# Optimization experiments

Measured on AMD Instinct MI355X. Metric: run time of the kernel, lower is better.

## Reference

```python
import jax, jax.numpy as jnp
import numpy as np

N_NODES = 100000
N_EDGES = 1600000
IN_CH = 256
OUT_CH = 128


def setup_inputs() -> dict:
    key = jax.random.key(0)
    k1, k2, k3, k4, k5, k6 = jax.random.split(key, 6)
    x = jax.random.normal(k1, (N_NODES, IN_CH), dtype=jnp.float32)
    edge_src = jax.random.randint(k2, (N_EDGES,), 0, N_NODES, dtype=jnp.int32)
    edge_dst = jax.random.randint(k3, (N_EDGES,), 0, N_NODES, dtype=jnp.int32)
    edge_weight = jax.random.uniform(k4, (N_EDGES,), dtype=jnp.float32)
    # Linear params (torch nn.Linear: y = x @ W.T + b)
    W = jax.random.normal(k5, (OUT_CH, IN_CH), dtype=jnp.float32) * (1.0 / np.sqrt(IN_CH))
    b = jax.random.normal(k6, (OUT_CH,), dtype=jnp.float32) * 0.01
    return {"x": x, "edge_src": edge_src, "edge_dst": edge_dst,
            "edge_weight": edge_weight, "W": W, "b": b}


def reference(x, edge_src, edge_dst, edge_weight, W, b):
    # Linear projection: [N, in] -> [N, out]
    h = x @ W.T + b
    # spmm sum aggregation: out[d] = sum_{e: dst(e)=d} w_e * h[src(e)]
    msgs = h[edge_src] * edge_weight[:, None]  # [E, out]
    out = jax.ops.segment_sum(msgs, edge_dst, num_segments=N_NODES)
    return out
```

## Files before the change

kernel.cpp:

```cpp
#include <hip/hip_runtime.h>
#include <hip/hip_bf16.h>

#define IN_CH 256
#define OUT_CH 128
#define BKT_SHIFT 7
#define BKT_SIZE 128
#define MAXNB 1024
#define K3_CHUNK 8192
#define MAXBLK 256
#define BATCH 3072
#define CAPP 4096

using bf16x8 = __attribute__((ext_vector_type(8))) __bf16;
using f32x16 = __attribute__((ext_vector_type(16))) float;
using f32x4  = __attribute__((ext_vector_type(4))) float;
using f32x2  = __attribute__((ext_vector_type(2))) float;

__device__ __forceinline__ unsigned int f2bf(float f) {
    union { float f; unsigned u; } v; v.f = f;
    unsigned r = v.u + 0x7fffu + ((v.u >> 16) & 1u);
    return r >> 16;
}
__device__ __forceinline__ float bf2f(unsigned short u) {
    union { unsigned u; float f; } v; v.u = ((unsigned)u) << 16;
    return v.f;
}

__global__ void __launch_bounds__(256) prep_w(const float* __restrict__ W,
                                              unsigned short* __restrict__ Wfrag) {
    const int flat = blockIdx.x * 256 + threadIdx.x;
    const int l = flat & 63;
    const int ks = (flat >> 6) & 15;
    const int c = flat >> 10;
    const int row = c * 32 + (l & 31);
    const int col0 = ks * 16 + 8 * (l >> 5);
    const float* src = W + (size_t)row * IN_CH + col0;
    uint4 o;
    o.x = f2bf(src[0]) | (f2bf(src[1]) << 16);
    o.y = f2bf(src[2]) | (f2bf(src[3]) << 16);
    o.z = f2bf(src[4]) | (f2bf(src[5]) << 16);
    o.w = f2bf(src[6]) | (f2bf(src[7]) << 16);
    *reinterpret_cast<uint4*>(Wfrag + (size_t)flat * 8) = o;
}

__global__ void __launch_bounds__(256) linear_mfma(
    const float* __restrict__ x, const unsigned short* __restrict__ Wfrag,
    const float* __restrict__ b, unsigned short* __restrict__ h, int n_nodes) {
    const int tid = threadIdx.x;
    const int w = tid >> 6, l = tid & 63;
    const int l31 = l & 31, lh = l >> 5;
    const int node0 = blockIdx.x * 128 + w * 32;

    int arow = node0 + l31;
    if (arow > n_nodes - 1) arow = n_nodes - 1;
    const float* xrow = x + (size_t)arow * IN_CH + 8 * lh;
    const uint4* wf = reinterpret_cast<const uint4*>(Wfrag);

    f32x16 acc0 = {}, acc1 = {}, acc2 = {}, acc3 = {};

#pragma unroll 4
    for (int ks = 0; ks < 16; ++ks) {
        float4 a0 = *reinterpret_cast<const float4*>(xrow + ks * 16);
        float4 a1 = *reinterpret_cast<const float4*>(xrow + ks * 16 + 4);
        bf16x8 af;
        af[0] = (__bf16)a0.x; af[1] = (__bf16)a0.y;
        af[2] = (__bf16)a0.z; af[3] = (__bf16)a0.w;
        af[4] = (__bf16)a1.x; af[5] = (__bf16)a1.y;
        af[6] = (__bf16)a1.z; af[7] = (__bf16)a1.w;

        uint4 bw0 = wf[(0 * 16 + ks) * 64 + l];
        uint4 bw1 = wf[(1 * 16 + ks) * 64 + l];
        uint4 bw2 = wf[(2 * 16 + ks) * 64 + l];
        uint4 bw3 = wf[(3 * 16 + ks) * 64 + l];

        acc0 = __builtin_amdgcn_mfma_f32_32x32x16_bf16(af, __builtin_bit_cast(bf16x8, bw0), acc0, 0, 0, 0);
        acc1 = __builtin_amdgcn_mfma_f32_32x32x16_bf16(af, __builtin_bit_cast(bf16x8, bw1), acc1, 0, 0, 0);
        acc2 = __builtin_amdgcn_mfma_f32_32x32x16_bf16(af, __builtin_bit_cast(bf16x8, bw2), acc2, 0, 0, 0);
        acc3 = __builtin_amdgcn_mfma_f32_32x32x16_bf16(af, __builtin_bit_cast(bf16x8, bw3), acc3, 0, 0, 0);
    }

    const float bias0 = b[0 + l31], bias1 = b[32 + l31], bias2 = b[64 + l31], bias3 = b[96 + l31];
#pragma unroll
    for (int reg = 0; reg < 16; ++reg) {
        const int r = (reg & 3) + 8 * (reg >> 2) + 4 * lh;
        const int node = node0 + r;
        if (node < n_nodes) {
            unsigned short* hp = h + (size_t)node * OUT_CH;
            __bf16 t0 = (__bf16)(acc0[reg] + bias0);
            __bf16 t1 = (__bf16)(acc1[reg] + bias1);
            __bf16 t2 = (__bf16)(acc2[reg] + bias2);
            __bf16 t3 = (__bf16)(acc3[reg] + bias3);
            hp[0 + l31]  = __builtin_bit_cast(unsigned short, t0);
            hp[32 + l31] = __builtin_bit_cast(unsigned short, t1);
            hp[64 + l31] = __builtin_bit_cast(unsigned short, t2);
            hp[96 + l31] = __builtin_bit_cast(unsigned short, t3);
        }
    }
}

__global__ void __launch_bounds__(512) k1_hist(
    const int* __restrict__ edge_dst, int* __restrict__ bh, int n_edges, int nb) {
    __shared__ int hist[MAXNB];
    const int t = threadIdx.x;
    const int blk = blockIdx.x;
    for (int i = t; i < MAXNB; i += 512) hist[i] = 0;
    __syncthreads();
    const int base = blk * K3_CHUNK;
#pragma unroll
    for (int j = 0; j < K3_CHUNK / 512; ++j) {
        int e = base + j * 512 + t;
        if (e < n_edges) atomicAdd(&hist[edge_dst[e] >> BKT_SHIFT], 1);
    }
    __syncthreads();
    for (int i = t; i < nb; i += 512) bh[i * MAXBLK + blk] = hist[i];
}

__global__ void __launch_bounds__(256) k2a_scan_cols(
    const int* __restrict__ bh, int* __restrict__ offs, int* __restrict__ total,
    int nblk) {
    __shared__ int sd[256];
    const int t = threadIdx.x;
    const int bkt = blockIdx.x;
    int val = (t < nblk) ? bh[bkt * MAXBLK + t] : 0;
    sd[t] = val;
    __syncthreads();
    for (int s = 1; s < 256; s <<= 1) {
        int y = (t >= s) ? sd[t - s] : 0;
        __syncthreads();
        sd[t] += y;
        __syncthreads();
    }
    offs[bkt * MAXBLK + t] = sd[t] - val;
    if (t == 255) total[bkt] = sd[255];
}

__global__ void __launch_bounds__(256) k2b_scan_base(
    const int* __restrict__ total, int* __restrict__ base, int nb) {
    __shared__ int sd[256];
    const int t = threadIdx.x;
    int v[4];
    int loc = 0;
#pragma unroll
    for (int k = 0; k < 4; ++k) {
        int idx = t * 4 + k;
        v[k] = (idx < nb) ? total[idx] : 0;
        loc += v[k];
    }
    sd[t] = loc;
    __syncthreads();
    for (int s = 1; s < 256; s <<= 1) {
        int y = (t >= s) ? sd[t - s] : 0;
        __syncthreads();
        sd[t] += y;
        __syncthreads();
    }
    int run = sd[t] - loc;
#pragma unroll
    for (int k = 0; k < 4; ++k) {
        int idx = t * 4 + k;
        if (idx < nb) base[idx] = run;
        run += v[k];
    }
    if (t == 255) base[nb] = sd[255];
}

__global__ void __launch_bounds__(512) k3_bin(
    const int* __restrict__ edge_src, const int* __restrict__ edge_dst,
    const float* __restrict__ edge_weight,
    const int* __restrict__ offs, const int* __restrict__ base,
    unsigned long long* __restrict__ records, int n_edges, int nb) {
    __shared__ unsigned long long staged[K3_CHUNK];
    __shared__ int hist[MAXNB];
    __shared__ int cur[MAXNB];
    __shared__ int gbase[MAXNB];
    __shared__ int sd[512];

    const int t = threadIdx.x;
    const int blk = blockIdx.x;
    const int ebase = blk * K3_CHUNK;
    const int count = min(K3_CHUNK, n_edges - ebase);

    for (int i = t; i < MAXNB; i += 512) hist[i] = 0;
    __syncthreads();
#pragma unroll
    for (int j = 0; j < K3_CHUNK / 512; ++j) {
        int e = ebase + j * 512 + t;
        if (e < n_edges) atomicAdd(&hist[edge_dst[e] >> BKT_SHIFT], 1);
    }
    __syncthreads();
    int h0 = hist[2 * t], h1 = hist[2 * t + 1];
    int loc = h0 + h1;
    sd[t] = loc;
    __syncthreads();
    for (int s = 1; s < 512; s <<= 1) {
        int y = (t >= s) ? sd[t - s] : 0;
        __syncthreads();
        sd[t] += y;
        __syncthreads();
    }
    int excl = sd[t] - loc;
    cur[2 * t] = excl;
    cur[2 * t + 1] = excl + h0;
    if (2 * t < nb)     gbase[2 * t]     = base[2 * t]     + offs[(2 * t) * MAXBLK + blk]     - excl;
    if (2 * t + 1 < nb) gbase[2 * t + 1] = base[2 * t + 1] + offs[(2 * t + 1) * MAXBLK + blk] - (excl + h0);
    __syncthreads();
#pragma unroll
    for (int j = 0; j < K3_CHUNK / 512; ++j) {
        int e = ebase + j * 512 + t;
        if (e < n_edges) {
            int d = edge_dst[e];
            int bkt = d >> BKT_SHIFT;
            unsigned int wbits = f2bf(edge_weight[e]);
            unsigned long long rec = ((unsigned long long)wbits << 48) |
                                     ((unsigned long long)bkt << 24) |
                                     ((unsigned long long)(d & (BKT_SIZE - 1)) << 17) |
                                     (unsigned int)edge_src[e];
            int pos = atomicAdd(&cur[bkt], 1);
            staged[pos] = rec;
        }
    }
    __syncthreads();
    for (int i = t; i < count; i += 512) {
        unsigned long long r = staged[i];
        int bkt = (int)((r >> 24) & 1023u);
        records[gbase[bkt] + i] = r;
    }
}

__global__ void __launch_bounds__(512) k4_agg(
    const unsigned short* __restrict__ h, const unsigned long long* __restrict__ records,
    const int* __restrict__ base, float* __restrict__ out, int n_nodes) {
    __shared__ unsigned long long sorted[CAPP];
    __shared__ int hist[BKT_SIZE];
    __shared__ int cur[BKT_SIZE];
    __shared__ int pstart[BKT_SIZE];
    __shared__ int sd[BKT_SIZE];
    __shared__ int ptot;

    const int t = threadIdx.x;
    const int bkt = blockIdx.x;
    const int w = t >> 6, lane = t & 63;
    const int rbeg = base[bkt], rend = base[bkt + 1];

    float acc[16][2];
#pragma unroll
    for (int d = 0; d < 16; ++d) { acc[d][0] = 0.f; acc[d][1] = 0.f; }

    for (int b0 = rbeg; b0 < rend; b0 += BATCH) {
        const int cnt = min(BATCH, rend - b0);
        __syncthreads();
        unsigned long long r[6];
#pragma unroll
        for (int j = 0; j < 6; ++j) {
            const int o = j * 512 + t;
            r[j] = (o < cnt) ? records[b0 + o] : 0ull;
        }
        if (t < BKT_SIZE) hist[t] = 0;
        __syncthreads();
#pragma unroll
        for (int j = 0; j < 6; ++j) {
            const int o = j * 512 + t;
            if (o < cnt) atomicAdd(&hist[(unsigned)(r[j] >> 17) & 127u], 1);
        }
        __syncthreads();
        if (t < BKT_SIZE) sd[t] = (hist[t] + 7) & ~7;
        __syncthreads();
        for (int s = 1; s < BKT_SIZE; s <<= 1) {
            int y = 0;
            if (t < BKT_SIZE && t >= s) y = sd[t - s];
            __syncthreads();
            if (t < BKT_SIZE) sd[t] += y;
            __syncthreads();
        }
        if (t < BKT_SIZE) {
            const int e = sd[t] - ((hist[t] + 7) & ~7);
            pstart[t] = e;
            cur[t] = e;
        }
        if (t == BKT_SIZE - 1) ptot = sd[BKT_SIZE - 1];
        __syncthreads();
        const int pt = ptot;
        for (int i = t; i < pt; i += 512) sorted[i] = 0ull;
        __syncthreads();
#pragma unroll
        for (int j = 0; j < 6; ++j) {
            const int o = j * 512 + t;
            if (o < cnt) {
                const int dl = (int)((unsigned)(r[j] >> 17) & 127u);
                const int pos = atomicAdd(&cur[dl], 1);
                sorted[pos] = r[j];
            }
        }
        __syncthreads();
#pragma unroll
        for (int d = 0; d < 16; ++d) {
            const int dl = w * 16 + d;
            const int s0 = pstart[dl];
            const int s1 = s0 + hist[dl];
            float a0 = 0.f, a1 = 0.f;
            for (int i = s0; i < s1; i += 8) {
                unsigned int hv[8];
                float wt[8];
#pragma unroll
                for (int j = 0; j < 8; ++j) {
                    const unsigned long long rr = sorted[i + j];
                    const unsigned lo = __builtin_amdgcn_readfirstlane((unsigned)rr);
                    const unsigned hi = __builtin_amdgcn_readfirstlane((unsigned)(rr >> 32));
                    wt[j] = __builtin_bit_cast(float, hi & 0xFFFF0000u);
                    const unsigned* hp = reinterpret_cast<const unsigned*>(
                        h + (size_t)(lo & 0x1FFFFu) * OUT_CH);
                    hv[j] = hp[lane];
                }
#pragma unroll
                for (int j = 0; j < 8; ++j) {
                    a0 += wt[j] * __builtin_bit_cast(float, hv[j] << 16);
                    a1 += wt[j] * __builtin_bit_cast(float, hv[j] & 0xFFFF0000u);
                }
            }
            acc[d][0] += a0;
            acc[d][1] += a1;
        }
    }

#pragma unroll
    for (int d = 0; d < 16; ++d) {
        const int node = bkt * BKT_SIZE + w * 16 + d;
        if (node < n_nodes) {
            f32x2 v = {acc[d][0], acc[d][1]};
            __builtin_nontemporal_store(
                v, reinterpret_cast<f32x2*>(out + (size_t)node * OUT_CH + 2 * lane));
        }
    }
}

extern "C" void kernel_launch(void* const* d_in, const int* in_sizes, int n_in,
                              void* d_out, int out_size, void* d_ws, size_t ws_size,
                              hipStream_t stream) {
    const float* x           = (const float*)d_in[0];
    const int*   edge_src    = (const int*)d_in[1];
    const int*   edge_dst    = (const int*)d_in[2];
    const float* edge_weight = (const float*)d_in[3];
    const float* W           = (const float*)d_in[4];
    const float* b           = (const float*)d_in[5];
    float* out = (float*)d_out;

    const int n_nodes = in_sizes[0] / IN_CH;
    const int n_edges = in_sizes[1];
    const int nb = (n_nodes + BKT_SIZE - 1) / BKT_SIZE;
    const int nblk = (n_edges + K3_CHUNK - 1) / K3_CHUNK;

    unsigned long long* records = (unsigned long long*)d_ws;
    unsigned short* h  = (unsigned short*)(records + n_edges);
    int* bh    = (int*)(h + (size_t)n_nodes * OUT_CH);
    int* offs  = bh + MAXNB * MAXBLK;
    int* total = offs + MAXNB * MAXBLK;
    int* base  = total + MAXNB;
    unsigned short* Wfrag = (unsigned short*)(base + MAXNB + 2);

    prep_w<<<16, 256, 0, stream>>>(W, Wfrag);
    linear_mfma<<<(n_nodes + 127) / 128, 256, 0, stream>>>(x, Wfrag, b, h, n_nodes);
    k1_hist<<<nblk, 512, 0, stream>>>(edge_dst, bh, n_edges, nb);
    k2a_scan_cols<<<nb, 256, 0, stream>>>(bh, offs, total, nblk);
    k2b_scan_base<<<1, 256, 0, stream>>>(total, base, nb);
    k3_bin<<<nblk, 512, 0, stream>>>(edge_src, edge_dst, edge_weight,
                                     offs, base, records, n_edges, nb);
    k4_agg<<<nb, 512, 0, stream>>>(h, records, base, out, n_nodes);
}
```

Baseline: 136.7 us.

## Split aggregation buckets across two blocks and stage W in LDS

The aggregation kernel now launches two blocks per 128-node bucket. Each block reads every record in the bucket but keeps only those whose destination falls in its 64-node half, which doubles the block count and parallelism at the cost of reading the records twice. The linear kernel moves to 512 threads and 256 nodes per block, and copies the 64 KB of W fragments into LDS once per block instead of loading them from global memory in every wave. The larger LDS footprint may limit how many linear blocks fit per CU.

```diff
diff --git a/kernel.cpp b/kernel.cpp
--- a/kernel.cpp
+++ b/kernel.cpp
@@ -5,6 +5,7 @@
 #define OUT_CH 128
 #define BKT_SHIFT 7
 #define BKT_SIZE 128
+#define BSUB 64
 #define MAXNB 1024
 #define K3_CHUNK 8192
 #define MAXBLK 256
@@ -43,18 +44,25 @@
     *reinterpret_cast<uint4*>(Wfrag + (size_t)flat * 8) = o;
 }
 
-__global__ void __launch_bounds__(256) linear_mfma(
+__global__ void __launch_bounds__(512) linear_mfma(
     const float* __restrict__ x, const unsigned short* __restrict__ Wfrag,
     const float* __restrict__ b, unsigned short* __restrict__ h, int n_nodes) {
+    __shared__ uint4 wlds[4096];
     const int tid = threadIdx.x;
     const int w = tid >> 6, l = tid & 63;
     const int l31 = l & 31, lh = l >> 5;
-    const int node0 = blockIdx.x * 128 + w * 32;
+    const int node0 = blockIdx.x * 256 + w * 32;
+
+    {
+        const uint4* wfg = reinterpret_cast<const uint4*>(Wfrag);
+#pragma unroll
+        for (int j = 0; j < 8; ++j) wlds[j * 512 + tid] = wfg[j * 512 + tid];
+    }
+    __syncthreads();
 
     int arow = node0 + l31;
     if (arow > n_nodes - 1) arow = n_nodes - 1;
     const float* xrow = x + (size_t)arow * IN_CH + 8 * lh;
-    const uint4* wf = reinterpret_cast<const uint4*>(Wfrag);
 
     f32x16 acc0 = {}, acc1 = {}, acc2 = {}, acc3 = {};
 
@@ -68,10 +76,10 @@
         af[4] = (__bf16)a1.x; af[5] = (__bf16)a1.y;
         af[6] = (__bf16)a1.z; af[7] = (__bf16)a1.w;
 
-        uint4 bw0 = wf[(0 * 16 + ks) * 64 + l];
-        uint4 bw1 = wf[(1 * 16 + ks) * 64 + l];
-        uint4 bw2 = wf[(2 * 16 + ks) * 64 + l];
-        uint4 bw3 = wf[(3 * 16 + ks) * 64 + l];
+        uint4 bw0 = wlds[(0 * 16 + ks) * 64 + l];
+        uint4 bw1 = wlds[(1 * 16 + ks) * 64 + l];
+        uint4 bw2 = wlds[(2 * 16 + ks) * 64 + l];
+        uint4 bw3 = wlds[(3 * 16 + ks) * 64 + l];
 
         acc0 = __builtin_amdgcn_mfma_f32_32x32x16_bf16(af, __builtin_bit_cast(bf16x8, bw0), acc0, 0, 0, 0);
         acc1 = __builtin_amdgcn_mfma_f32_32x32x16_bf16(af, __builtin_bit_cast(bf16x8, bw1), acc1, 0, 0, 0);
@@ -231,70 +239,71 @@
     const unsigned short* __restrict__ h, const unsigned long long* __restrict__ records,
     const int* __restrict__ base, float* __restrict__ out, int n_nodes) {
     __shared__ unsigned long long sorted[CAPP];
-    __shared__ int hist[BKT_SIZE];
-    __shared__ int cur[BKT_SIZE];
-    __shared__ int pstart[BKT_SIZE];
-    __shared__ int sd[BKT_SIZE];
+    __shared__ int hist[BSUB];
+    __shared__ int cur[BSUB];
+    __shared__ int pstart[BSUB];
+    __shared__ int sd[BSUB];
     __shared__ int ptot;
 
     const int t = threadIdx.x;
-    const int bkt = blockIdx.x;
+    const int bkt = blockIdx.x >> 1;
+    const int sub = blockIdx.x & 1;
     const int w = t >> 6, lane = t & 63;
     const int rbeg = base[bkt], rend = base[bkt + 1];
 
-    float acc[16][2];
-#pragma unroll
-    for (int d = 0; d < 16; ++d) { acc[d][0] = 0.f; acc[d][1] = 0.f; }
+    float acc[8][2];
+#pragma unroll
+    for (int d = 0; d < 8; ++d) { acc[d][0] = 0.f; acc[d][1] = 0.f; }
 
     for (int b0 = rbeg; b0 < rend; b0 += BATCH) {
         const int cnt = min(BATCH, rend - b0);
         __syncthreads();
         unsigned long long r[6];
+        int keep[6];
 #pragma unroll
         for (int j = 0; j < 6; ++j) {
             const int o = j * 512 + t;
             r[j] = (o < cnt) ? records[b0 + o] : 0ull;
-        }
-        if (t < BKT_SIZE) hist[t] = 0;
-        __syncthreads();
-#pragma unroll
-        for (int j = 0; j < 6; ++j) {
-            const int o = j * 512 + t;
-            if (o < cnt) atomicAdd(&hist[(unsigned)(r[j] >> 17) & 127u], 1);
-        }
-        __syncthreads();
-        if (t < BKT_SIZE) sd[t] = (hist[t] + 7) & ~7;
-        __syncthreads();
-        for (int s = 1; s < BKT_SIZE; s <<= 1) {
+            const int dl7 = (int)((unsigned)(r[j] >> 17) & 127u);
+            keep[j] = (o < cnt) && ((dl7 >> 6) == sub);
+        }
+        if (t < BSUB) hist[t] = 0;
+        __syncthreads();
+#pragma unroll
+        for (int j = 0; j < 6; ++j)
+            if (keep[j]) atomicAdd(&hist[(unsigned)(r[j] >> 17) & 63u], 1);
+        __syncthreads();
+        if (t < BSUB) sd[t] = (hist[t] + 7) & ~7;
+        __syncthreads();
+        for (int s = 1; s < BSUB; s <<= 1) {
             int y = 0;
-            if (t < BKT_SIZE && t >= s) y = sd[t - s];
+            if (t < BSUB && t >= s) y = sd[t - s];
             __syncthreads();
-            if (t < BKT_SIZE) sd[t] += y;
+            if (t < BSUB) sd[t] += y;
             __syncthreads();
         }
-        if (t < BKT_SIZE) {
+        if (t < BSUB) {
             const int e = sd[t] - ((hist[t] + 7) & ~7);
             pstart[t] = e;
             cur[t] = e;
         }
-        if (t == BKT_SIZE - 1) ptot = sd[BKT_SIZE - 1];
+        if (t == BSUB - 1) ptot = sd[BSUB - 1];
         __syncthreads();
         const int pt = ptot;
         for (int i = t; i < pt; i += 512) sorted[i] = 0ull;
         __syncthreads();
 #pragma unroll
         for (int j = 0; j < 6; ++j) {
-            const int o = j * 512 + t;
-            if (o < cnt) {
-                const int dl = (int)((unsigned)(r[j] >> 17) & 127u);
+            if (keep[j]) {
+                const int dl = (int)((unsigned)(r[j] >> 17) & 63u);
                 const int pos = atomicAdd(&cur[dl], 1);
                 sorted[pos] = r[j];
             }
         }
         __syncthreads();
 #pragma unroll
-        for (int d = 0; d < 16; ++d) {
-            const int dl = w * 16 + d;
+        for (int d = 0; d < 8; ++d) {
+            const int dl = w * 8 + d;
             const int s0 = pstart[dl];
             const int s1 = s0 + hist[dl];
             float a0 = 0.f, a1 = 0.f;
@@ -323,8 +332,8 @@
     }
 
 #pragma unroll
-    for (int d = 0; d < 16; ++d) {
-        const int node = bkt * BKT_SIZE + w * 16 + d;
+    for (int d = 0; d < 8; ++d) {
+        const int node = bkt * BKT_SIZE + sub * BSUB + w * 8 + d;
         if (node < n_nodes) {
             f32x2 v = {acc[d][0], acc[d][1]};
             __builtin_nontemporal_store(
@@ -358,11 +367,11 @@
     unsigned short* Wfrag = (unsigned short*)(base + MAXNB + 2);
 
     prep_w<<<16, 256, 0, stream>>>(W, Wfrag);
-    linear_mfma<<<(n_nodes + 127) / 128, 256, 0, stream>>>(x, Wfrag, b, h, n_nodes);
+    linear_mfma<<<(n_nodes + 255) / 256, 512, 0, stream>>>(x, Wfrag, b, h, n_nodes);
     k1_hist<<<nblk, 512, 0, stream>>>(edge_dst, bh, n_edges, nb);
     k2a_scan_cols<<<nb, 256, 0, stream>>>(bh, offs, total, nblk);
     k2b_scan_base<<<1, 256, 0, stream>>>(total, base, nb);
     k3_bin<<<nblk, 512, 0, stream>>>(edge_src, edge_dst, edge_weight,
                                      offs, base, records, n_edges, nb);
-    k4_agg<<<nb, 512, 0, stream>>>(h, records, base, out, n_nodes);
-}
+    k4_agg<<<nb * 2, 512, 0, stream>>>(h, records, base, out, n_nodes);
+}
```

Result: faster. 130.6 us (-4.4%).
